# Kernel tuning notes

Hardware: AMD Instinct MI355X
Metric: run time of the kernel (lower is better)

The kernel has to match this reference:

```python
import jax, jax.numpy as jnp
import numpy as np

CD_WEIGHT = 1.0
EMD_WEIGHT = 1.0
EPS = 1e-3        # sinkhorn entropic regularization (matches eps=0.001)
ITERS = 50        # matches max_iters=50 (stop_thresh ignored: fixed trip count for jit)
NEG = -1e9        # log(0) stand-in for padded points
BIG = 1e10        # +inf stand-in for masked chamfer distances


def _sqdist(x, y):
    # x [N,3], y [M,3] -> squared euclidean distances [N,M]  (p=2 cost)
    return jnp.maximum(
        jnp.sum(x * x, -1)[:, None] + jnp.sum(y * y, -1)[None, :] - 2.0 * (x @ y.T),
        0.0,
    )


def _sinkhorn_cost(x, y, n, m):
    # Log-domain Sinkhorn OT cost between one padded pair: x [N,3], y [M,3],
    # with n, m valid points and uniform marginals 1/n, 1/m on valid points.
    N, M = x.shape[0], y.shape[0]
    C = _sqdist(x, y)
    nf = n.astype(jnp.float32)
    mf = m.astype(jnp.float32)
    log_a = jnp.where(jnp.arange(N) < n, -jnp.log(nf), NEG)  # [N]
    log_b = jnp.where(jnp.arange(M) < m, -jnp.log(mf), NEG)  # [M]

    def body(_, fg):
        f, g = fg
        f = -EPS * jax.scipy.special.logsumexp(log_b[None, :] + (g[None, :] - C) / EPS, axis=1)
        g = -EPS * jax.scipy.special.logsumexp(log_a[:, None] + (f[:, None] - C) / EPS, axis=0)
        return (f, g)

    f, g = jax.lax.fori_loop(0, ITERS, body, (jnp.zeros(N), jnp.zeros(M)))
    log_P = log_a[:, None] + log_b[None, :] + (f[:, None] + g[None, :] - C) / EPS
    return jnp.sum(jnp.exp(log_P) * C)


def _chamfer(px, gy, n_len, m_len):
    # pytorch3d chamfer_distance with point_reduction='mean', batch_reduction='mean'
    # px [B,N,3], gy [B,M,3]; n_len/m_len [B] float valid counts.
    B, N, _ = px.shape
    M = gy.shape[1]
    D = jnp.maximum(
        jnp.sum(px * px, -1)[:, :, None]
        + jnp.sum(gy * gy, -1)[:, None, :]
        - 2.0 * jnp.einsum('bnd,bmd->bnm', px, gy),
        0.0,
    )  # [B,N,M]
    mx = jnp.arange(N)[None, :] < n_len[:, None]  # [B,N]
    my = jnp.arange(M)[None, :] < m_len[:, None]  # [B,M]
    dx = jnp.min(jnp.where(my[:, None, :], D, BIG), axis=2)  # [B,N] NN dist x->y
    dy = jnp.min(jnp.where(mx[:, :, None], D, BIG), axis=1)  # [B,M] NN dist y->x
    cham_x = jnp.sum(jnp.where(mx, dx, 0.0), axis=1) / n_len.astype(jnp.float32)
    cham_y = jnp.sum(jnp.where(my, dy, 0.0), axis=1) / m_len.astype(jnp.float32)
    return jnp.mean(cham_x + cham_y)


def setup_inputs() -> dict:
    key = jax.random.key(0)
    k1, k2, k3, k4 = jax.random.split(key, 4)
    B, N, M = 8, 2048, 2048
    pred_points = 0.5 * jax.random.normal(k1, (B, N, 3), dtype=jnp.float32)
    gt_points = 0.5 * jax.random.normal(k2, (B, M, 3), dtype=jnp.float32)
    pred_lengths = jax.random.randint(k3, (B,), N // 2, N + 1, dtype=jnp.int32)
    gt_lengths = jax.random.randint(k4, (B,), M // 2, M + 1, dtype=jnp.int32)
    return {
        'pred_points': pred_points,
        'gt_points': gt_points,
        'pred_lengths': pred_lengths,
        'gt_lengths': gt_lengths,
    }


def reference(pred_points, gt_points, pred_lengths, gt_lengths):
    # Original clips extracted points to [-1, 1] before losses.
    px = jnp.clip(pred_points, -1.0, 1.0)
    gy = jnp.clip(gt_points, -1.0, 1.0)
    # EMD: per-sample sinkhorn cost, sqrt, mean over samples, weighted.
    emd_costs = jax.vmap(_sinkhorn_cost)(px, gy, pred_lengths, gt_lengths)  # [B]
    emd_loss = EMD_WEIGHT * jnp.mean(jnp.sqrt(emd_costs))
    # Chamfer on padded clouds with lengths.
    cd_loss = CD_WEIGHT * _chamfer(px, gy, pred_lengths.astype(jnp.float32), gt_lengths.astype(jnp.float32))
    return cd_loss + emd_loss
```

## Files before the change

kernel.cpp:

```cpp
#include <hip/hip_runtime.h>

#define BATCH 8
#define NPTS  2048
#define TPB   512
#define WGB   64
#define NWG   (BATCH*WGB)
#define ITERS 50
#define R     4

#define KLOG2E    1442.6950408889634f
#define TWO_K     2885.3900817779268f
#define INV_TK    3.4657359027997264e-4f
#define INV_K     6.931471805599453e-4f
#define INV_2K_SQ 1.2011325347955035e-7f
#define AR_SCALE  -1.7328679513998632e-4f
#define NEGU      -1e30f
#define BIGD      1e10f

typedef float f2 __attribute__((ext_vector_type(2)));

__device__ __forceinline__ float exp2fast(float x) { return __builtin_amdgcn_exp2f(x); }
__device__ __forceinline__ float log2fast(float x) { return __builtin_amdgcn_logf(x); }
__device__ __forceinline__ float clipf(float v)    { return fminf(fmaxf(v, -1.0f), 1.0f); }
__device__ __forceinline__ f2 bc(float x) { f2 r; r.x = x; r.y = x; return r; }

__device__ __forceinline__ f2 pk_fma(f2 a, f2 b, f2 c) {
    f2 d;
    asm("v_pk_fma_f32 %0, %1, %2, %3" : "=v"(d) : "v"(a), "v"(b), "v"(c));
    return d;
}
__device__ __forceinline__ f2 pk_add(f2 a, f2 b) {
    f2 d;
    asm("v_pk_add_f32 %0, %1, %2" : "=v"(d) : "v"(a), "v"(b));
    return d;
}

__device__ __forceinline__ float aloadf(const float* p) {
    return __hip_atomic_load(p, __ATOMIC_RELAXED, __HIP_MEMORY_SCOPE_AGENT);
}
__device__ __forceinline__ void astoref(float* p, float v) {
    __hip_atomic_store(p, v, __ATOMIC_RELAXED, __HIP_MEMORY_SCOPE_AGENT);
}
__device__ __forceinline__ int aloadi(const int* p) {
    return __hip_atomic_load(p, __ATOMIC_RELAXED, __HIP_MEMORY_SCOPE_AGENT);
}
__device__ __forceinline__ void astorei(int* p, int v) {
    __hip_atomic_store(p, v, __ATOMIC_RELAXED, __HIP_MEMORY_SCOPE_AGENT);
}
__device__ __forceinline__ f2 aloadf2(const float* p) {
    unsigned long long v = __hip_atomic_load((const unsigned long long*)p,
                                             __ATOMIC_RELAXED, __HIP_MEMORY_SCOPE_AGENT);
    union { unsigned long long u; f2 f; } c; c.u = v; return c.f;
}

__device__ __forceinline__ float wsum(float v) {
#pragma unroll
    for (int d = 1; d < 64; d <<= 1) v += __shfl_xor(v, d);
    return v;
}
__device__ __forceinline__ float wmax(float v) {
#pragma unroll
    for (int d = 1; d < 64; d <<= 1) v = fmaxf(v, __shfl_xor(v, d));
    return v;
}
__device__ __forceinline__ float wmin(float v) {
#pragma unroll
    for (int d = 1; d < 64; d <<= 1) v = fminf(v, __shfl_xor(v, d));
    return v;
}

__device__ __forceinline__ bool half_fused_pk(
    const f2* __restrict__ cx, const f2* __restrict__ cy,
    const f2* __restrict__ cz, const f2* __restrict__ cw,
    const f2* __restrict__ rx, const f2* __restrict__ ry, const f2* __restrict__ rz,
    float L2C, float* L, float* D, float* uv,
    int nrows, int ncols, int r0, int lane)
{
    if (r0 >= nrows) return false;
    const int nst = (ncols + 127) >> 7;
    const int rp = r0 >> 1;
    f2 vx0 = rx[rp], vx1 = rx[rp + 1];
    f2 vy0 = ry[rp], vy1 = ry[rp + 1];
    f2 vz0 = rz[rp], vz1 = rz[rp + 1];
    f2 x0p[R] = { bc(vx0.x * INV_TK), bc(vx0.y * INV_TK), bc(vx1.x * INV_TK), bc(vx1.y * INV_TK) };
    f2 x1p[R] = { bc(vy0.x * INV_TK), bc(vy0.y * INV_TK), bc(vy1.x * INV_TK), bc(vy1.y * INV_TK) };
    f2 x2p[R] = { bc(vz0.x * INV_TK), bc(vz0.y * INV_TK), bc(vz1.x * INV_TK), bc(vz1.y * INV_TK) };

    float Lp[R];
    f2 nLp[R];
#pragma unroll
    for (int r = 0; r < R; ++r) { Lp[r] = L[r] + D[r]; nLp[r] = bc(-Lp[r]); }

    float S0[R], S1[R];
#pragma unroll
    for (int r = 0; r < R; ++r) { S0[r] = 0.0f; S1[r] = 0.0f; }

    for (int s = 0; s < nst; ++s) {
        int p = (s << 6) + lane;
        f2 bx = cx[p], by = cy[p], bz = cz[p], bw = cw[p];
#pragma unroll
        for (int r = 0; r < R; ++r) {
            f2 t = pk_fma(x2p[r], bz, bw);
            t = pk_fma(x1p[r], by, t);
            t = pk_fma(x0p[r], bx, t);
            t = pk_add(nLp[r], t);
            S0[r] += exp2fast(t.x);
            S1[r] += exp2fast(t.y);
        }
    }

    float Ssum[R];
    bool redo = false;
#pragma unroll
    for (int r = 0; r < R; ++r) {
        Ssum[r] = wsum(S0[r] + S1[r]);
        redo |= !(Ssum[r] >= 1e-30f && Ssum[r] <= 1e30f);
    }
    if (redo) {
        float Mn[R];
#pragma unroll
        for (int r = 0; r < R; ++r) Mn[r] = -3.0e38f;
        for (int s = 0; s < nst; ++s) {
            int p = (s << 6) + lane;
            f2 bx = cx[p], by = cy[p], bz = cz[p], bw = cw[p];
#pragma unroll
            for (int r = 0; r < R; ++r) {
                f2 t = pk_fma(x2p[r], bz, bw);
                t = pk_fma(x1p[r], by, t);
                t = pk_fma(x0p[r], bx, t);
                Mn[r] = fmaxf(Mn[r], fmaxf(t.x, t.y));
            }
        }
#pragma unroll
        for (int r = 0; r < R; ++r) {
            Lp[r] = wmax(Mn[r]); nLp[r] = bc(-Lp[r]);
            S0[r] = 0.0f; S1[r] = 0.0f;
        }
        for (int s = 0; s < nst; ++s) {
            int p = (s << 6) + lane;
            f2 bx = cx[p], by = cy[p], bz = cz[p], bw = cw[p];
#pragma unroll
            for (int r = 0; r < R; ++r) {
                f2 t = pk_fma(x2p[r], bz, bw);
                t = pk_fma(x1p[r], by, t);
                t = pk_fma(x0p[r], bx, t);
                t = pk_add(nLp[r], t);
                S0[r] += exp2fast(t.x);
                S1[r] += exp2fast(t.y);
            }
        }
#pragma unroll
        for (int r = 0; r < R; ++r) Ssum[r] = wsum(S0[r] + S1[r]);
    }

#pragma unroll
    for (int r = 0; r < R; ++r) {
        float lnew = Lp[r] + log2fast(Ssum[r]);
        D[r] = (L[r] > 1.0e37f) ? 0.0f : (lnew - L[r]);
        L[r] = lnew;
        uv[r] = L2C - lnew;
    }
    return true;
}

__launch_bounds__(TPB, 4)
__global__ void pcl_kernel(const float* __restrict__ pred,
                           const float* __restrict__ gt,
                           const int* __restrict__ nlen,
                           const int* __restrict__ mlen,
                           int* __restrict__ hdr,
                           float* __restrict__ fbuf,
                           float* __restrict__ gbuf,
                           float* __restrict__ parts,
                           float* __restrict__ bres,
                           float* __restrict__ out)
{
    __shared__ f2 XSX[NPTS/2], XSY[NPTS/2], XSZ[NPTS/2];
    __shared__ f2 YSX[NPTS/2], YSY[NPTS/2], YSZ[NPTS/2];
    __shared__ float4 WBUF[TPB];

    const int tid  = threadIdx.x;
    const int wg   = blockIdx.x;
    const int lo   = wg & 255;
    const int hi   = wg >> 8;
    const int b    = ((lo & 7) + hi) & 7;
    const int wloc = (lo >> 3) + hi * 32;
    const int wv   = tid >> 6;
    const int lane = tid & 63;
    const int r0   = wloc * 32 + wv * R;
    const int rg   = wloc * 8 + wv;
    const int j0   = tid << 2;
    const int n = nlen[b];
    const int m = mlen[b];
    const float nf = (float)n, mf = (float)m;
    const float* predb = pred + (size_t)b * NPTS * 3;
    const float* gtb   = gt   + (size_t)b * NPTS * 3;
    float* fb = fbuf + b * NPTS;
    float* gb = gbuf + b * NPTS;
    int* flagF = hdr + b * 512;
    int* flagG = hdr + 4096 + b * 512;
    int* cntb  = hdr + 8192 + b * 16;
    int* done  = hdr + 8320;

    for (int idx = tid; idx < NPTS; idx += TPB) {
        const float* p = predb + (size_t)idx * 3;
        ((float*)XSX)[idx] = clipf(p[0]) * TWO_K;
        ((float*)XSY)[idx] = clipf(p[1]) * TWO_K;
        ((float*)XSZ)[idx] = clipf(p[2]) * TWO_K;
        const float* q = gtb + (size_t)idx * 3;
        ((float*)YSX)[idx] = clipf(q[0]) * TWO_K;
        ((float*)YSY)[idx] = clipf(q[1]) * TWO_K;
        ((float*)YSZ)[idx] = clipf(q[2]) * TWO_K;
    }
    __syncthreads();

    const float L2M = log2fast(mf);
    const float L2N = log2fast(nf);

    float Lf[R], Lg[R], Df[R], Dg[R];
#pragma unroll
    for (int r = 0; r < R; ++r) {
        Lf[r] = 3.0e38f; Lg[r] = 3.0e38f;
        Df[r] = 0.0f;    Dg[r] = 0.0f;
    }
    float uv[R];

    for (int it = 0; it < ITERS; ++it) {
        {
            float4 w;
            if (it == 0) {
                f2 gx0 = YSX[2*tid],   gy0 = YSY[2*tid],   gz0 = YSZ[2*tid];
                f2 gx1 = YSX[2*tid+1], gy1 = YSY[2*tid+1], gz1 = YSZ[2*tid+1];
                f2 s0 = gx0*gx0 + gy0*gy0 + gz0*gz0;
                f2 s1 = gx1*gx1 + gy1*gy1 + gz1*gz1;
                w.x = s0.x * AR_SCALE; w.y = s0.y * AR_SCALE;
                w.z = s1.x * AR_SCALE; w.w = s1.y * AR_SCALE;
            } else {
                if (j0 < m) {
                    const int* fp = &flagG[j0 >> 2];
                    while (aloadi(fp) < it) __builtin_amdgcn_s_sleep(2);
                }
                asm volatile("" ::: "memory");
                f2 a = aloadf2(&gb[j0]);
                f2 c = aloadf2(&gb[j0 + 2]);
                w.x = a.x; w.y = a.y; w.z = c.x; w.w = c.y;
            }
            if (j0 + 3 >= m) {
                if (j0     >= m) w.x = NEGU;
                if (j0 + 1 >= m) w.y = NEGU;
                if (j0 + 2 >= m) w.z = NEGU;
                w.w = NEGU;
            }
            WBUF[tid] = w;
        }
        __syncthreads();
        if (half_fused_pk(YSX, YSY, YSZ, (const f2*)WBUF, XSX, XSY, XSZ,
                          L2M, Lf, Df, uv, n, m, r0, lane)) {
            float v = uv[0];
#pragma unroll
            for (int r = 1; r < R; ++r) v = (lane == r) ? uv[r] : v;
            if (lane < R && (r0 + lane) < n) astoref(&fb[r0 + lane], v);
            asm volatile("s_waitcnt vmcnt(0)" ::: "memory");
            if (lane == 0) astorei(&flagF[rg], it + 1);
        }
        __syncthreads();

        {
            if (j0 < n) {
                const int* fp = &flagF[j0 >> 2];
                while (aloadi(fp) < it + 1) __builtin_amdgcn_s_sleep(2);
            }
            asm volatile("" ::: "memory");
            f2 a = aloadf2(&fb[j0]);
            f2 c = aloadf2(&fb[j0 + 2]);
            float4 w;
            w.x = a.x; w.y = a.y; w.z = c.x; w.w = c.y;
            if (j0 + 3 >= n) {
                if (j0     >= n) w.x = NEGU;
                if (j0 + 1 >= n) w.y = NEGU;
                if (j0 + 2 >= n) w.z = NEGU;
                w.w = NEGU;
            }
            WBUF[tid] = w;
        }
        __syncthreads();
        if (half_fused_pk(XSX, XSY, XSZ, (const f2*)WBUF, YSX, YSY, YSZ,
                          L2N, Lg, Dg, uv, m, n, r0, lane)) {
            float v = uv[0];
#pragma unroll
            for (int r = 1; r < R; ++r) v = (lane == r) ? uv[r] : v;
            if (lane < R && (r0 + lane) < m) astoref(&gb[r0 + lane], v);
            asm volatile("s_waitcnt vmcnt(0)" ::: "memory");
            if (lane == 0) astorei(&flagG[rg], it + 1);
        }
        __syncthreads();
    }

    {
        if (j0 < m) {
            const int* fp = &flagG[j0 >> 2];
            while (aloadi(fp) < ITERS) __builtin_amdgcn_s_sleep(2);
        }
        asm volatile("" ::: "memory");
        f2 a = aloadf2(&gb[j0]);
        f2 c = aloadf2(&gb[j0 + 2]);
        float4 w;
        w.x = a.x; w.y = a.y; w.z = c.x; w.w = c.y;
        if (j0 + 3 >= m) {
            if (j0     >= m) w.x = NEGU;
            if (j0 + 1 >= m) w.y = NEGU;
            if (j0 + 2 >= m) w.z = NEGU;
            w.w = NEGU;
        }
        WBUF[tid] = w;
    }
    __syncthreads();

    float wcost = 0.0f, chx = 0.0f;
    if (r0 < n) {
        const f2* YWf = (const f2*)WBUF;
        const int rp = r0 >> 1;
        f2 vx0 = XSX[rp], vx1 = XSX[rp + 1];
        f2 vy0 = XSY[rp], vy1 = XSY[rp + 1];
        f2 vz0 = XSZ[rp], vz1 = XSZ[rp + 1];
        float px0[R] = { vx0.x * INV_TK, vx0.y * INV_TK, vx1.x * INV_TK, vx1.y * INV_TK };
        float px1[R] = { vy0.x * INV_TK, vy0.y * INV_TK, vy1.x * INV_TK, vy1.y * INV_TK };
        float px2[R] = { vz0.x * INV_TK, vz0.y * INV_TK, vz1.x * INV_TK, vz1.y * INV_TK };
        float pxx[R], hrow[R];
        f2 dmn[R];
#pragma unroll
        for (int r = 0; r < R; ++r) {
            float sx = px0[r] * TWO_K, sy = px1[r] * TWO_K, sz = px2[r] * TWO_K;
            pxx[r] = fmaf(sx, sx, fmaf(sy, sy, sz * sz)) * INV_2K_SQ;
            hrow[r] = (r0 + r < n) ? aloadf(&fb[r0 + r]) : NEGU;
            dmn[r].x = BIGD; dmn[r].y = BIGD;
        }
        const int nst = (m + 127) >> 7;
        for (int s = 0; s < nst; ++s) {
            int p = (s << 6) + lane;
            f2 bx = YSX[p], by = YSY[p], bz = YSZ[p], bw = YWf[p];
            f2 yy2 = (bx * bx + by * by + bz * bz) * INV_2K_SQ;
            bool jv0 = (2 * p)     < m;
            bool jv1 = (2 * p + 1) < m;
#pragma unroll
            for (int r = 0; r < R; ++r) {
                f2 dots = px0[r] * bx + px1[r] * by + px2[r] * bz;
                f2 e = dots + bw + hrow[r];
                float w0 = exp2fast(e.x), w1 = exp2fast(e.y);
                f2 C;
                C.x = fmaxf(fmaf(dots.x, -INV_K, pxx[r] + yy2.x), 0.0f);
                C.y = fmaxf(fmaf(dots.y, -INV_K, pxx[r] + yy2.y), 0.0f);
                wcost = fmaf(w0, C.x, fmaf(w1, C.y, wcost));
                dmn[r].x = fminf(dmn[r].x, jv0 ? C.x : BIGD);
                dmn[r].y = fminf(dmn[r].y, jv1 ? C.y : BIGD);
            }
        }
#pragma unroll
        for (int r = 0; r < R; ++r) {
            float d = wmin(fminf(dmn[r].x, dmn[r].y));
            if (r0 + r < n) chx += d;
        }
        wcost = wsum(wcost);
    }

    float chy = 0.0f;
    if (r0 < m) {
        const int rp = r0 >> 1;
        f2 vx0 = YSX[rp], vx1 = YSX[rp + 1];
        f2 vy0 = YSY[rp], vy1 = YSY[rp + 1];
        f2 vz0 = YSZ[rp], vz1 = YSZ[rp + 1];
        float qy0[R] = { vx0.x * INV_TK, vx0.y * INV_TK, vx1.x * INV_TK, vx1.y * INV_TK };
        float qy1[R] = { vy0.x * INV_TK, vy0.y * INV_TK, vy1.x * INV_TK, vy1.y * INV_TK };
        float qy2[R] = { vz0.x * INV_TK, vz0.y * INV_TK, vz1.x * INV_TK, vz1.y * INV_TK };
        float qyy[R];
        f2 dmn[R];
#pragma unroll
        for (int r = 0; r < R; ++r) {
            float sx = qy0[r] * TWO_K, sy = qy1[r] * TWO_K, sz = qy2[r] * TWO_K;
            qyy[r] = fmaf(sx, sx, fmaf(sy, sy, sz * sz)) * INV_2K_SQ;
            dmn[r].x = BIGD; dmn[r].y = BIGD;
        }
        const int nst = (n + 127) >> 7;
        for (int s = 0; s < nst; ++s) {
            int p = (s << 6) + lane;
            f2 bx = XSX[p], by = XSY[p], bz = XSZ[p];
            f2 xx2 = (bx * bx + by * by + bz * bz) * INV_2K_SQ;
            bool iv0 = (2 * p)     < n;
            bool iv1 = (2 * p + 1) < n;
#pragma unroll
            for (int r = 0; r < R; ++r) {
                f2 dots = qy0[r] * bx + qy1[r] * by + qy2[r] * bz;
                f2 C;
                C.x = fmaxf(fmaf(dots.x, -INV_K, qyy[r] + xx2.x), 0.0f);
                C.y = fmaxf(fmaf(dots.y, -INV_K, qyy[r] + xx2.y), 0.0f);
                dmn[r].x = fminf(dmn[r].x, iv0 ? C.x : BIGD);
                dmn[r].y = fminf(dmn[r].y, iv1 ? C.y : BIGD);
            }
        }
#pragma unroll
        for (int r = 0; r < R; ++r) {
            float d = wmin(fminf(dmn[r].x, dmn[r].y));
            if (r0 + r < m) chy += d;
        }
    }
    __syncthreads();

    float* xs = (float*)XSX;
    if (lane == 0) { xs[wv] = wcost; xs[8 + wv] = chx; xs[16 + wv] = chy; }
    __syncthreads();
    if (tid == 0) {
        float cs = 0.0f, cx = 0.0f, cy = 0.0f;
        for (int w = 0; w < 8; ++w) { cs += xs[w]; cx += xs[8 + w]; cy += xs[16 + w]; }
        astoref(&parts[(b * WGB + wloc) * 4 + 0], cs);
        astoref(&parts[(b * WGB + wloc) * 4 + 1], cx);
        astoref(&parts[(b * WGB + wloc) * 4 + 2], cy);
        asm volatile("s_waitcnt vmcnt(0)" ::: "memory");
        __hip_atomic_fetch_add(cntb, 1, __ATOMIC_RELAXED, __HIP_MEMORY_SCOPE_AGENT);
    }

    if (wloc == 0 && wv == 0) {
        while (aloadi(cntb) < WGB) __builtin_amdgcn_s_sleep(2);
        asm volatile("" ::: "memory");
        float cs = aloadf(&parts[(b * WGB + lane) * 4 + 0]);
        float cx = aloadf(&parts[(b * WGB + lane) * 4 + 1]);
        float cy = aloadf(&parts[(b * WGB + lane) * 4 + 2]);
        cs = wsum(cs); cx = wsum(cx); cy = wsum(cy);
        if (lane == 0) {
            float cost = cs / (nf * mf);
            astoref(&bres[b], sqrtf(fmaxf(cost, 0.0f)) + cx / nf + cy / mf);
            asm volatile("s_waitcnt vmcnt(0)" ::: "memory");
            int a = __hip_atomic_fetch_add(done, 1, __ATOMIC_RELAXED, __HIP_MEMORY_SCOPE_AGENT);
            if (a == BATCH - 1) {
                float acc = 0.0f;
                for (int i2 = 0; i2 < BATCH; ++i2) acc += aloadf(&bres[i2]);
                out[0] = acc * 0.125f;
            }
        }
    }
}

extern "C" void kernel_launch(void* const* d_in, const int* in_sizes, int n_in,
                              void* d_out, int out_size, void* d_ws, size_t ws_size,
                              hipStream_t stream) {
    const float* pred = (const float*)d_in[0];
    const float* gt   = (const float*)d_in[1];
    const int*  nlen  = (const int*)d_in[2];
    const int*  mlen  = (const int*)d_in[3];

    int*   hdr   = (int*)d_ws;
    float* base  = (float*)d_ws + 9216;
    float* fbuf  = base;
    float* gbuf  = fbuf + BATCH * NPTS;
    float* parts = gbuf + BATCH * NPTS;
    float* bres  = parts + NWG * 4;
    float* out   = (float*)d_out;

    hipMemsetAsync(d_ws, 0, 36864, stream);
    hipLaunchKernelGGL(pcl_kernel, dim3(NWG), dim3(TPB), 0, stream,
                       pred, gt, nlen, mlen, hdr, fbuf, gbuf, parts, bres, out);
}
```

Baseline: 896.3 us.

## Poll cross-workgroup flags with a single wave and double-buffer LDS weights

Per-thread spin-waits on individual global flags are replaced by a single wave that polls every flag with a wave-wide all-reduce, followed by a workgroup barrier. Separate LDS buffers for the X and Y potential vectors let one trailing barrier per iteration be removed. The aim is less polling traffic on global memory from all threads and fewer barriers. In exchange, every thread now waits for all rows to be ready instead of only its own group, which can add latency.

```diff
diff --git a/kernel.cpp b/kernel.cpp
--- a/kernel.cpp
+++ b/kernel.cpp
@@ -67,6 +67,23 @@
 #pragma unroll
     for (int d = 1; d < 64; d <<= 1) v = fminf(v, __shfl_xor(v, d));
     return v;
+}
+
+__device__ __forceinline__ void wavepoll(const int* __restrict__ flags,
+                                         int target, int cntv, int wv, int lane)
+{
+    if (wv != 0) return;
+    for (;;) {
+        int mn = target;
+#pragma unroll
+        for (int k = 0; k < 8; ++k) {
+            int idx = lane + (k << 6);
+            int v = (idx < cntv) ? aloadi(&flags[idx]) : target;
+            mn = min(mn, v);
+        }
+        if (__all(mn >= target)) break;
+        __builtin_amdgcn_s_sleep(2);
+    }
 }
 
 __device__ __forceinline__ bool half_fused_pk(
@@ -177,7 +194,7 @@
 {
     __shared__ f2 XSX[NPTS/2], XSY[NPTS/2], XSZ[NPTS/2];
     __shared__ f2 YSX[NPTS/2], YSY[NPTS/2], YSZ[NPTS/2];
-    __shared__ float4 WBUF[TPB];
+    __shared__ float4 XW[TPB], YW[TPB];
 
     const int tid  = threadIdx.x;
     const int wg   = blockIdx.x;
@@ -193,6 +210,8 @@
     const int n = nlen[b];
     const int m = mlen[b];
     const float nf = (float)n, mf = (float)m;
+    const int cvn = (n + 3) >> 2;
+    const int cvm = (m + 3) >> 2;
     const float* predb = pred + (size_t)b * NPTS * 3;
     const float* gtb   = gt   + (size_t)b * NPTS * 3;
     float* fb = fbuf + b * NPTS;
@@ -226,6 +245,8 @@
     float uv[R];
 
     for (int it = 0; it < ITERS; ++it) {
+        if (it > 0) wavepoll(flagG, it, cvm, wv, lane);
+        __syncthreads();
         {
             float4 w;
             if (it == 0) {
@@ -236,11 +257,6 @@
                 w.x = s0.x * AR_SCALE; w.y = s0.y * AR_SCALE;
                 w.z = s1.x * AR_SCALE; w.w = s1.y * AR_SCALE;
             } else {
-                if (j0 < m) {
-                    const int* fp = &flagG[j0 >> 2];
-                    while (aloadi(fp) < it) __builtin_amdgcn_s_sleep(2);
-                }
-                asm volatile("" ::: "memory");
                 f2 a = aloadf2(&gb[j0]);
                 f2 c = aloadf2(&gb[j0 + 2]);
                 w.x = a.x; w.y = a.y; w.z = c.x; w.w = c.y;
@@ -251,10 +267,10 @@
                 if (j0 + 2 >= m) w.z = NEGU;
                 w.w = NEGU;
             }
-            WBUF[tid] = w;
+            YW[tid] = w;
         }
         __syncthreads();
-        if (half_fused_pk(YSX, YSY, YSZ, (const f2*)WBUF, XSX, XSY, XSZ,
+        if (half_fused_pk(YSX, YSY, YSZ, (const f2*)YW, XSX, XSY, XSZ,
                           L2M, Lf, Df, uv, n, m, r0, lane)) {
             float v = uv[0];
 #pragma unroll
@@ -263,14 +279,10 @@
             asm volatile("s_waitcnt vmcnt(0)" ::: "memory");
             if (lane == 0) astorei(&flagF[rg], it + 1);
         }
+
+        wavepoll(flagF, it + 1, cvn, wv, lane);
         __syncthreads();
-
         {
-            if (j0 < n) {
-                const int* fp = &flagF[j0 >> 2];
-                while (aloadi(fp) < it + 1) __builtin_amdgcn_s_sleep(2);
-            }
-            asm volatile("" ::: "memory");
             f2 a = aloadf2(&fb[j0]);
             f2 c = aloadf2(&fb[j0 + 2]);
             float4 w;
@@ -281,10 +293,10 @@
                 if (j0 + 2 >= n) w.z = NEGU;
                 w.w = NEGU;
             }
-            WBUF[tid] = w;
+            XW[tid] = w;
         }
         __syncthreads();
-        if (half_fused_pk(XSX, XSY, XSZ, (const f2*)WBUF, YSX, YSY, YSZ,
+        if (half_fused_pk(XSX, XSY, XSZ, (const f2*)XW, YSX, YSY, YSZ,
                           L2N, Lg, Dg, uv, m, n, r0, lane)) {
             float v = uv[0];
 #pragma unroll
@@ -293,15 +305,11 @@
             asm volatile("s_waitcnt vmcnt(0)" ::: "memory");
             if (lane == 0) astorei(&flagG[rg], it + 1);
         }
-        __syncthreads();
-    }
-
+    }
+
+    wavepoll(flagG, ITERS, cvm, wv, lane);
+    __syncthreads();
     {
-        if (j0 < m) {
-            const int* fp = &flagG[j0 >> 2];
-            while (aloadi(fp) < ITERS) __builtin_amdgcn_s_sleep(2);
-        }
-        asm volatile("" ::: "memory");
         f2 a = aloadf2(&gb[j0]);
         f2 c = aloadf2(&gb[j0 + 2]);
         float4 w;
@@ -312,13 +320,13 @@
             if (j0 + 2 >= m) w.z = NEGU;
             w.w = NEGU;
         }
-        WBUF[tid] = w;
+        YW[tid] = w;
     }
     __syncthreads();
 
     float wcost = 0.0f, chx = 0.0f;
     if (r0 < n) {
-        const f2* YWf = (const f2*)WBUF;
+        const f2* YWf = (const f2*)YW;
         const int rp = r0 >> 1;
         f2 vx0 = XSX[rp], vx1 = XSX[rp + 1];
         f2 vy0 = XSY[rp], vy1 = XSY[rp + 1];
```

Result: slower. 970.8 us (+8.3%).
